# Performance work log

Hardware: AMD Instinct MI355X
Metric: run time of the kernel (lower is better)

## Reference

```python
import jax, jax.numpy as jnp
import numpy as np

B, S, D = 2, 2048, 2048
H = 16
NOPE, ROPE, DV = 128, 64, 128
DQK = NOPE + ROPE  # 192
QLR, KVLR = 1536, 512


def setup_inputs() -> dict:
    key = jax.random.key(0)
    ks = jax.random.split(key, 8)
    hidden_states = jax.random.normal(ks[0], (B, S, D), dtype=jnp.float32) * 0.02
    sequence_mask = jnp.ones((B, S), dtype=bool)
    # rotary frequencies (complex exponential split into cos/sin), theta=10000
    inv_freq = 1.0 / (10000.0 ** (np.arange(0, ROPE, 2, dtype=np.float32) / ROPE))
    angles = np.outer(np.arange(S, dtype=np.float32), inv_freq)  # [S, ROPE//2]
    freqs_cos = jnp.asarray(np.cos(angles), dtype=jnp.float32)
    freqs_sin = jnp.asarray(np.sin(angles), dtype=jnp.float32)
    def lin(k, fan_in, fan_out):
        return jax.random.normal(k, (fan_in, fan_out), dtype=jnp.float32) / np.sqrt(fan_in)
    return {
        'hidden_states': hidden_states,
        'sequence_mask': sequence_mask,
        'freqs_cos': freqs_cos,
        'freqs_sin': freqs_sin,
        'Wq_down': lin(ks[1], D, QLR),
        'Wkv_down': lin(ks[2], D, KVLR + ROPE),
        'Wq_up': lin(ks[3], QLR, H * DQK),
        'Wkv_up': lin(ks[4], KVLR, H * (DV + NOPE)),
        'Wo': lin(ks[5], H * DV, D),
    }


def _rmsnorm(x, eps=1e-5):
    return x * jax.lax.rsqrt(jnp.mean(x * x, axis=-1, keepdims=True) + eps)


def _apply_rope(x, cos, sin):
    # x: [B,S,H,d] with interleaved (real, imag) pairs; cos/sin: [S, d//2]
    b, s, h, d = x.shape
    xr = x.reshape(b, s, h, d // 2, 2)
    x0, x1 = xr[..., 0], xr[..., 1]
    c = cos[None, :s, None, :]
    sn = sin[None, :s, None, :]
    y = jnp.stack([x0 * c - x1 * sn, x0 * sn + x1 * c], axis=-1)
    return y.reshape(b, s, h, d)


def reference(hidden_states, sequence_mask, freqs_cos, freqs_sin,
              Wq_down, Wkv_down, Wq_up, Wkv_up, Wo):
    b, s, _ = hidden_states.shape
    # Q path: down-project -> rmsnorm -> up-project
    q_latent = _rmsnorm(hidden_states @ Wq_down)
    q = (q_latent @ Wq_up).reshape(b, s, H, DQK)
    q_nope, q_rope = q[..., :NOPE], q[..., NOPE:]
    q_rope = _apply_rope(q_rope, freqs_cos, freqs_sin)
    q = jnp.concatenate([q_rope, q_nope], axis=-1)  # [B,S,H,DQK]
    # KV path
    kvdr = hidden_states @ Wkv_down  # [B,S,KVLR+ROPE]
    kv_latent, k_rope = kvdr[..., :KVLR], kvdr[..., KVLR:]
    k_rope = _apply_rope(k_rope.reshape(b, s, 1, ROPE), freqs_cos, freqs_sin)
    k_rope = jnp.broadcast_to(k_rope, (b, s, H, ROPE))
    kv = _rmsnorm(kv_latent) @ Wkv_up  # [B,S,H*(NOPE+DV)]
    k_nope = kv[..., :H * NOPE].reshape(b, s, H, NOPE)
    v = kv[..., H * NOPE:].reshape(b, s, H, DV)
    k = jnp.concatenate([k_rope, k_nope], axis=-1)  # [B,S,H,DQK]
    # causal attention (flash_attn_varlen with full masks == per-batch causal)
    scale = 1.0 / np.sqrt(DQK)
    scores = jnp.einsum('bqhd,bkhd->bhqk', q, k) * scale
    causal = jnp.tril(jnp.ones((s, s), dtype=bool))
    mask = causal[None, None, :, :] & sequence_mask[:, None, None, :]
    scores = jnp.where(mask, scores, jnp.float32(-1e9))
    attn = jax.nn.softmax(scores, axis=-1)
    out = jnp.einsum('bhqk,bkhd->bqhd', attn, v).reshape(b, s, H * DV)
    return out @ Wo
```

## Files before the change

### kernel.cpp

```cpp
#include <hip/hip_runtime.h>
#include <math.h>


typedef unsigned short u16;
typedef __attribute__((ext_vector_type(8))) __bf16 bf16x8;
typedef __attribute__((ext_vector_type(4))) float f32x4;

#define DEV static __device__ __forceinline__

#if __has_builtin(__builtin_amdgcn_exp2f)
#define EXP2(x) __builtin_amdgcn_exp2f(x)
#else
#define EXP2(x) exp2f(x)
#endif

DEV float b2f(u16 v) { return __uint_as_float(((unsigned int)v) << 16); }
DEV u16 f2b(float f) {
  unsigned int u = __float_as_uint(f);
  u += 0x7fffu + ((u >> 16) & 1u);
  return (u16)(u >> 16);
}
DEV u16 f2b_hw(float f) {
  __bf16 h = (__bf16)f;
  u16 r;
  __builtin_memcpy(&r, &h, 2);
  return r;
}

DEV float waveReduceSum(float v) {
  #pragma unroll
  for (int o = 32; o > 0; o >>= 1) v += __shfl_down(v, o, 64);
  return v;
}

DEV void gld16(const u16* g, u16* l) {
  __builtin_amdgcn_global_load_lds((const __attribute__((address_space(1))) void*)g,
                                   (__attribute__((address_space(3))) void*)l, 16, 0, 0);
}

__global__ __launch_bounds__(256)
void cvt_f32_bf16(const float* __restrict__ in, u16* __restrict__ out, int n4) {
  int i = blockIdx.x * 256 + threadIdx.x;
  if (i < n4) {
    float4 v = reinterpret_cast<const float4*>(in)[i];
    ushort4 o;
    o.x = f2b(v.x); o.y = f2b(v.y); o.z = f2b(v.z); o.w = f2b(v.w);
    reinterpret_cast<ushort4*>(out)[i] = o;
  }
}

__global__ __launch_bounds__(256)
void transpose_all(const float* __restrict__ Wqd, const float* __restrict__ Wkvd,
                   const float* __restrict__ Wqu, const float* __restrict__ Wkvu,
                   const float* __restrict__ Wo,
                   u16* __restrict__ W13T, u16* __restrict__ WquT,
                   u16* __restrict__ WkvuT, u16* __restrict__ WoT) {
  __shared__ u16 tile[32][33];
  int n = blockIdx.x;
  const float* in; u16* out; int R, C, gx, local;
  if (n < 3072)       { in = Wqd;  out = W13T;                        R = 2048; C = 1536; gx = 48;  local = n; }
  else if (n < 4224)  { in = Wkvd; out = W13T + (size_t)1536 * 2048;  R = 2048; C = 576;  gx = 18;  local = n - 3072; }
  else if (n < 8832)  { in = Wqu;  out = WquT;                        R = 1536; C = 3072; gx = 96;  local = n - 4224; }
  else if (n < 10880) { in = Wkvu; out = WkvuT;                       R = 512;  C = 4096; gx = 128; local = n - 8832; }
  else                { in = Wo;   out = WoT;                         R = 2048; C = 2048; gx = 64;  local = n - 10880; }
  int c0 = (local % gx) * 32, r0 = (local / gx) * 32;
  for (int i = threadIdx.y; i < 32; i += 8)
    tile[i][threadIdx.x] = f2b(in[(size_t)(r0 + i) * C + c0 + threadIdx.x]);
  __syncthreads();
  for (int i = threadIdx.y; i < 32; i += 8)
    out[(size_t)(c0 + i) * R + r0 + threadIdx.x] = tile[threadIdx.x][i];
}

template<int OUT_BF16>
DEV void gemm8_body(const u16* __restrict__ A, const u16* __restrict__ BT, void* __restrict__ Cp,
                    int N, int K, int gx, int nwg, int orig,
                    u16 (*As)[8192], u16 (*Bs)[4096]) {
  const int tid = threadIdx.x;
  const int lane = tid & 63;
  const int wave = tid >> 6;
  const int wm = (wave >> 1) * 64;
  const int wn = (wave & 1) * 64;
  const int q = lane >> 4;
  const int l16 = lane & 15;

  const int cpx = nwg >> 3;
  const int swz = (orig & 7) * cpx + (orig >> 3);
  const int bm = (swz / gx) * 256;
  const int bn = (swz % gx) * 128;

  auto stageA = [&](int buf, int k0) {
    #pragma unroll
    for (int i = 0; i < 2; i++) {
      int ub = i * 512 + wave * 64;
      int u = ub + lane;
      int row = u >> 2;
      int kq = (u & 3) ^ ((u >> 3) & 3);
      gld16(A + (size_t)(bm + row) * K + k0 + kq * 8, As[buf] + ub * 8);
    }
  };
  auto stageB = [&](int buf, int k0) {
    int ub = wave * 64;
    int u = ub + lane;
    int row = u >> 2;
    int kq = (u & 3) ^ ((u >> 3) & 3);
    int rB = bn + row;
    if (rB >= N) rB = N - 1;
    gld16(BT + (size_t)rB * K + k0 + kq * 8, Bs[buf] + ub * 8);
  };

  f32x4 zero = {0.f, 0.f, 0.f, 0.f};
  f32x4 acc[4][4];
  #pragma unroll
  for (int i = 0; i < 4; i++)
    #pragma unroll
    for (int j = 0; j < 4; j++) acc[i][j] = zero;

  const int nt = K >> 5;
  stageA(0, 0);  stageB(0, 0);
  stageA(1, 32); stageB(1, 32);

  for (int t = 0; t < nt; ++t) {
    const int cur = t % 3;
    if (t + 1 < nt) asm volatile("s_waitcnt vmcnt(3)" ::: "memory");
    else            asm volatile("s_waitcnt vmcnt(0)" ::: "memory");
    __builtin_amdgcn_sched_barrier(0);
    __builtin_amdgcn_s_barrier();
    __builtin_amdgcn_sched_barrier(0);

    const u16* Ab = As[cur];
    const u16* Bb = Bs[cur];
    const int nxt = (t + 2) % 3;
    const bool pre = (t + 2) < nt;
    const int kpre = (t + 2) * 32;

    bf16x8 af[4], bfr[4];
    #pragma unroll
    for (int j = 0; j < 4; j++) {
      int rowA = wm + j * 16 + l16;
      af[j]  = *reinterpret_cast<const bf16x8*>(Ab + (((rowA) << 2) | (q ^ ((rowA >> 1) & 3))) * 8);
      int rowB = wn + j * 16 + l16;
      bfr[j] = *reinterpret_cast<const bf16x8*>(Bb + (((rowB) << 2) | (q ^ ((rowB >> 1) & 3))) * 8);
    }
    if (pre) { stageA(nxt, kpre); stageB(nxt, kpre); }
    __builtin_amdgcn_s_setprio(1);
    #pragma unroll
    for (int mt = 0; mt < 4; mt++)
      #pragma unroll
      for (int j = 0; j < 4; j++)
        acc[mt][j] = __builtin_amdgcn_mfma_f32_16x16x32_bf16(af[mt], bfr[j], acc[mt][j], 0, 0, 0);
    __builtin_amdgcn_s_setprio(0);
  }

  float* Cf = (float*)Cp;
  u16* Cb = (u16*)Cp;
  #pragma unroll
  for (int mt = 0; mt < 4; mt++) {
    #pragma unroll
    for (int j = 0; j < 4; j++) {
      int col = bn + wn + j * 16 + l16;
      if (col < N) {
        int row0 = bm + wm + mt * 16 + q * 4;
        #pragma unroll
        for (int r = 0; r < 4; r++) {
          size_t idx = (size_t)(row0 + r) * N + col;
          float v = acc[mt][j][r];
          if (OUT_BF16) Cb[idx] = f2b(v); else Cf[idx] = v;
        }
      }
    }
  }
}

template<int OUT_BF16>
__global__ __launch_bounds__(512, 4)
void gemm8(const u16* __restrict__ A, const u16* __restrict__ BT, void* __restrict__ Cp,
           int N, int K) {
  __shared__ __attribute__((aligned(16))) u16 As[3][8192];
  __shared__ __attribute__((aligned(16))) u16 Bs[3][4096];
  const int gx = gridDim.x;
  const int nwg = gx * gridDim.y;
  const int orig = blockIdx.y * gx + blockIdx.x;
  gemm8_body<OUT_BF16>(A, BT, Cp, N, K, gx, nwg, orig, As, Bs);
}

__global__ __launch_bounds__(512, 4)
void gemm_up2(const u16* __restrict__ qlat, const u16* __restrict__ WquT, u16* __restrict__ q2,
              const u16* __restrict__ kvl, const u16* __restrict__ WkvuT, u16* __restrict__ kvb) {
  __shared__ __attribute__((aligned(16))) u16 As[3][8192];
  __shared__ __attribute__((aligned(16))) u16 Bs[3][4096];
  int n = blockIdx.x;
  if (n < 384) gemm8_body<1>(qlat, WquT, q2, 3072, 1536, 24, 384, n, As, Bs);
  else         gemm8_body<1>(kvl, WkvuT, kvb, 4096, 512, 32, 512, n - 384, As, Bs);
}

__global__ __launch_bounds__(256)
void norm_split(const float* __restrict__ t13, const float* __restrict__ fc, const float* __restrict__ fs,
                u16* __restrict__ qlat, u16* __restrict__ kvl, u16* __restrict__ krope) {
  __shared__ float red[4];
  __shared__ float s_scale;
  int lane = threadIdx.x & 63, wid = threadIdx.x >> 6;
  if (blockIdx.x < 4096) {
    int row = blockIdx.x;
    const float* x = t13 + (size_t)row * 2112;
    float ss = 0.f;
    for (int i = threadIdx.x; i < 1536; i += 256) { float v = x[i]; ss += v * v; }
    ss = waveReduceSum(ss);
    if (lane == 0) red[wid] = ss;
    __syncthreads();
    if (threadIdx.x == 0)
      s_scale = rsqrtf((red[0] + red[1] + red[2] + red[3]) * (1.0f / 1536.0f) + 1e-5f);
    __syncthreads();
    float sc = s_scale;
    u16* o = qlat + (size_t)row * 1536;
    for (int i = threadIdx.x; i < 1536; i += 256) o[i] = f2b(x[i] * sc);
  } else {
    int row = blockIdx.x - 4096;
    int s = row & 2047;
    const float* x = t13 + (size_t)row * 2112 + 1536;
    float ss = 0.f;
    for (int i = threadIdx.x; i < 512; i += 256) { float v = x[i]; ss += v * v; }
    ss = waveReduceSum(ss);
    if (lane == 0) red[wid] = ss;
    __syncthreads();
    if (threadIdx.x == 0)
      s_scale = rsqrtf((red[0] + red[1] + red[2] + red[3]) * (1.0f / 512.0f) + 1e-5f);
    __syncthreads();
    float sc = s_scale;
    for (int i = threadIdx.x; i < 512; i += 256) kvl[(size_t)row * 512 + i] = f2b(x[i] * sc);
    if (threadIdx.x < 32) {
      int i = threadIdx.x;
      float cc = fc[s * 32 + i], sn = fs[s * 32 + i];
      float x0 = x[512 + 2 * i], x1 = x[512 + 2 * i + 1];
      krope[(size_t)row * 64 + 2 * i]     = f2b(x0 * cc - x1 * sn);
      krope[(size_t)row * 64 + 2 * i + 1] = f2b(x0 * sn + x1 * cc);
    }
  }
}

__global__ __launch_bounds__(256)
void rope_pack_q(const u16* __restrict__ q2, const float* __restrict__ fc, const float* __restrict__ fs,
                 u16* __restrict__ Q) {
  const float scale = 0.10411756711f;
  int bs = blockIdx.x;
  int b = bs >> 11, s = bs & 2047;
  __shared__ float c[32], sn[32];
  if (threadIdx.x < 32) {
    c[threadIdx.x] = fc[s * 32 + threadIdx.x];
    sn[threadIdx.x] = fs[s * 32 + threadIdx.x];
  }
  __syncthreads();
  const u16* qrow = q2 + (size_t)bs * 3072;
  for (int t = threadIdx.x; t < 512; t += 256) {
    int h = t >> 5, i = t & 31;
    float x0 = b2f(qrow[h * 192 + 128 + 2 * i]);
    float x1 = b2f(qrow[h * 192 + 128 + 2 * i + 1]);
    size_t base = ((size_t)(b * 16 + h) * 2048 + s) * 192;
    Q[base + 2 * i]     = f2b((x0 * c[i] - x1 * sn[i]) * scale);
    Q[base + 2 * i + 1] = f2b((x0 * sn[i] + x1 * c[i]) * scale);
  }
  for (int t = threadIdx.x; t < 2048; t += 256) {
    int h = t >> 7, j = t & 127;
    Q[((size_t)(b * 16 + h) * 2048 + s) * 192 + 64 + j] = f2b(b2f(qrow[h * 192 + j]) * scale);
  }
}

__global__ __launch_bounds__(256)
void assemble_kv2(const u16* __restrict__ kvb, const u16* __restrict__ krope,
                  u16* __restrict__ Kc, u16* __restrict__ Vt) {
  int ks = blockIdx.x;
  int bh = blockIdx.y;
  int b = bh >> 4, h = bh & 15;
  int t = threadIdx.x;
  if (t < 192) {
    int kq = t >> 3, sl = t & 7;
    int s = ks * 8 + sl;
    size_t bs = (size_t)(b * 2048 + s);
    uint4 v;
    if (kq < 8) v = *reinterpret_cast<const uint4*>(krope + bs * 64 + kq * 8);
    else        v = *reinterpret_cast<const uint4*>(kvb + bs * 4096 + h * 128 + (kq - 8) * 8);
    *reinterpret_cast<uint4*>(Kc + (((size_t)bh * 24 + kq) * 2048 + s) * 8) = v;
  }
  if (t < 128) {
    int dv = t;
    u16 tmp[8];
    #pragma unroll
    for (int j = 0; j < 8; j++) {
      int s = ks * 8 + j;
      tmp[j] = kvb[(size_t)(b * 2048 + s) * 4096 + 2048 + h * 128 + dv];
    }
    *reinterpret_cast<uint4*>(Vt + (((size_t)bh * 256 + ks) * 128 + dv) * 8) = *reinterpret_cast<uint4*>(tmp);
  }
}

__global__ __launch_bounds__(256, 2)
void flash_attn8(const u16* __restrict__ Q, const u16* __restrict__ Kc,
                 const u16* __restrict__ Vt, u16* __restrict__ O) {
  __shared__ __attribute__((aligned(16))) u16 Ks[2][24 * 64 * 8];
  __shared__ __attribute__((aligned(16))) u16 Vs[8 * 128 * 8];
  __shared__ __attribute__((aligned(16))) u16 Ps[4 * 16 * 72];

  const int blk = blockIdx.x;
  const int bh = ((blk & 7) << 2) | (blk >> 7);
  const int tpair = (blk >> 3) & 15;
  const int b = bh >> 4, h = bh & 15;
  const int tid = threadIdx.x, lane = tid & 63, wave = tid >> 6;
  const int quad = lane >> 4, l16 = lane & 15;
  u16* PsW = Ps + wave * 16 * 72;

  bf16x8 onesf;
  #pragma unroll
  for (int j = 0; j < 8; j++) onesf[j] = (l16 == 0) ? (__bf16)1.0f : (__bf16)0.0f;

  auto stageK = [&](u16* KsB, int kk) {
    #pragma unroll
    for (int ii = 0; ii < 6; ii++) {
      int kq = wave * 6 + ii;
      gld16(Kc + (((size_t)bh * 24 + kq) * 2048 + kk + lane) * 8, KsB + kq * 64 * 8);
    }
  };
  auto stageV = [&](int kk) {
    #pragma unroll
    for (int jj = 0; jj < 4; jj++) {
      int vc = wave * 4 + jj, kc = vc >> 1, dvh = vc & 1;
      gld16(Vt + (((size_t)bh * 256 + (kk >> 3) + kc) * 128 + dvh * 64 + lane) * 8,
            Vs + (kc * 128 + dvh * 64) * 8);
    }
  };

  for (int phase = 0; phase < 2; phase++) {
    const int qt = phase == 0 ? tpair : 31 - tpair;
    const int q0 = qt * 64;
    const int nk = (qt + 1) * 64;

    bf16x8 qf[6];
    {
      int qrow = q0 + wave * 16 + l16;
      const u16* qp = Q + ((size_t)bh * 2048 + qrow) * 192 + quad * 8;
      #pragma unroll
      for (int kc = 0; kc < 6; kc++)
        qf[kc] = *reinterpret_cast<const bf16x8*>(qp + kc * 32);
    }

    f32x4 zero = {0.f, 0.f, 0.f, 0.f};
    f32x4 oacc[9];
    #pragma unroll
    for (int nt = 0; nt < 9; nt++) oacc[nt] = zero;

    for (int k0 = 0; k0 < nk; k0 += 64) {
      const int cur = (k0 >> 6) & 1;
      const bool hasnext = (k0 + 64 < nk);

      __builtin_amdgcn_s_barrier();
      __builtin_amdgcn_sched_barrier(0);
      if (k0 == 0) stageK(Ks[0], 0);
      stageV(k0);
      if (hasnext) {
        stageK(Ks[cur ^ 1], k0 + 64);
        asm volatile("s_waitcnt vmcnt(10)" ::: "memory");
      } else {
        asm volatile("s_waitcnt vmcnt(4)" ::: "memory");
      }
      __builtin_amdgcn_sched_barrier(0);
      __builtin_amdgcn_s_barrier();
      __builtin_amdgcn_sched_barrier(0);

      const u16* KsC = Ks[cur];

      f32x4 sacc[4];
      #pragma unroll
      for (int nt = 0; nt < 4; nt++) sacc[nt] = zero;
      #pragma unroll
      for (int kc = 0; kc < 6; kc++) {
        #pragma unroll
        for (int nt = 0; nt < 4; nt++) {
          bf16x8 kb = *reinterpret_cast<const bf16x8*>(KsC + ((kc * 4 + quad) * 64 + nt * 16 + l16) * 8);
          sacc[nt] = __builtin_amdgcn_mfma_f32_16x16x32_bf16(qf[kc], kb, sacc[nt], 0, 0, 0);
        }
      }

      if (k0 + 63 <= q0 + wave * 16) {
        #pragma unroll
        for (int r = 0; r < 4; r++) {
          #pragma unroll
          for (int nt = 0; nt < 4; nt++) {
            float p = EXP2(sacc[nt][r]);
            PsW[(quad * 4 + r) * 72 + nt * 16 + l16] = f2b_hw(p);
          }
        }
      } else {
        #pragma unroll
        for (int r = 0; r < 4; r++) {
          int qrow_g = q0 + wave * 16 + quad * 4 + r;
          #pragma unroll
          for (int nt = 0; nt < 4; nt++) {
            int key = k0 + nt * 16 + l16;
            float e = EXP2(sacc[nt][r]);
            float p = (key <= qrow_g) ? e : 0.f;
            PsW[(quad * 4 + r) * 72 + nt * 16 + l16] = f2b_hw(p);
          }
        }
      }

      if (hasnext) asm volatile("s_waitcnt vmcnt(6)" ::: "memory");
      else         asm volatile("s_waitcnt vmcnt(0)" ::: "memory");
      __builtin_amdgcn_sched_barrier(0);
      __builtin_amdgcn_s_barrier();
      __builtin_amdgcn_sched_barrier(0);

      #pragma unroll
      for (int kcp = 0; kcp < 2; kcp++) {
        bf16x8 pa = *reinterpret_cast<const bf16x8*>(PsW + l16 * 72 + kcp * 32 + quad * 8);
        #pragma unroll
        for (int nt = 0; nt < 8; nt++) {
          bf16x8 vb = *reinterpret_cast<const bf16x8*>(Vs + ((kcp * 4 + quad) * 128 + nt * 16 + l16) * 8);
          oacc[nt] = __builtin_amdgcn_mfma_f32_16x16x32_bf16(pa, vb, oacc[nt], 0, 0, 0);
        }
        oacc[8] = __builtin_amdgcn_mfma_f32_16x16x32_bf16(pa, onesf, oacc[8], 0, 0, 0);
      }
    }

    #pragma unroll
    for (int r = 0; r < 4; r++) {
      float l = __shfl(oacc[8][r], lane & 48, 64);
      float inv = 1.0f / l;
      int s = q0 + wave * 16 + quad * 4 + r;
      #pragma unroll
      for (int nt = 0; nt < 8; nt++)
        O[((size_t)b * 2048 + s) * 2048 + h * 128 + nt * 16 + l16] = f2b(oacc[nt][r] * inv);
    }
  }
}

extern "C" void kernel_launch(void* const* d_in, const int* in_sizes, int n_in,
                              void* d_out, int out_size, void* d_ws, size_t ws_size,
                              hipStream_t stream) {
  (void)in_sizes; (void)n_in; (void)out_size; (void)ws_size;
  const float* hs   = (const float*)d_in[0];
  const float* fc   = (const float*)d_in[2];
  const float* fs   = (const float*)d_in[3];
  const float* Wqd  = (const float*)d_in[4];
  const float* Wkvd = (const float*)d_in[5];
  const float* Wqu  = (const float*)d_in[6];
  const float* Wkvu = (const float*)d_in[7];
  const float* Wo   = (const float*)d_in[8];

  char* ws = (char*)d_ws;
  size_t off = 0;
  auto alloc = [&](size_t bytes) { size_t o = off; off += (bytes + 255) & ~(size_t)255; return o; };
  const size_t oHS   = alloc(16777216);
  const size_t oRA   = alloc(16777216);
  const size_t oRB   = alloc(25165824);
  const size_t oRC   = alloc(12582912);
  const size_t oRD   = alloc(25165824);
  const size_t oRE   = alloc(34603008);
  const size_t oKVL  = alloc(4194304);
  const size_t oKR   = alloc(524288);
  const size_t oW13T  = alloc(8650752);
  const size_t oWquT  = alloc(9437184);
  const size_t oWkvuT = alloc(4194304);
  const size_t oWoT   = alloc(8388608);

  u16* hs_bf = (u16*)(ws + oHS);
  u16* Vt   = (u16*)(ws + oRA);
  u16* q2   = (u16*)(ws + oRB);
  u16* Kc   = (u16*)(ws + oRB);
  u16* qlat = (u16*)(ws + oRC);
  u16* Qb   = (u16*)(ws + oRD);
  float* t13 = (float*)(ws + oRE);
  u16* kvb  = (u16*)(ws + oRE);
  u16* attn_out = (u16*)(ws + oRE);
  u16* kvl  = (u16*)(ws + oKVL);
  u16* krope = (u16*)(ws + oKR);
  u16* W13T  = (u16*)(ws + oW13T);
  u16* WquT  = (u16*)(ws + oWquT);
  u16* WkvuT = (u16*)(ws + oWkvuT);
  u16* WoT   = (u16*)(ws + oWoT);

  cvt_f32_bf16<<<8192, 256, 0, stream>>>(hs, hs_bf, 2097152);
  transpose_all<<<14976, dim3(32, 8), 0, stream>>>(Wqd, Wkvd, Wqu, Wkvu, Wo, W13T, WquT, WkvuT, WoT);

  gemm8<0><<<dim3(17, 16), 512, 0, stream>>>(hs_bf, W13T, t13, 2112, 2048);
  norm_split<<<8192, 256, 0, stream>>>(t13, fc, fs, qlat, kvl, krope);
  gemm_up2<<<896, 512, 0, stream>>>(qlat, WquT, q2, kvl, WkvuT, kvb);
  rope_pack_q<<<4096, 256, 0, stream>>>(q2, fc, fs, Qb);
  assemble_kv2<<<dim3(256, 32), 256, 0, stream>>>(kvb, krope, Kc, Vt);
  flash_attn8<<<dim3(512), 256, 0, stream>>>(Qb, Kc, Vt, attn_out);
  gemm8<0><<<dim3(16, 16), 512, 0, stream>>>(attn_out, WoT, (float*)d_out, 2048, 2048);
}
```

Measured before the change: 412.9 us.

## Process both causal query tiles in one shared key loop in flash attention

Each block previously handled its two paired query tiles (short and long) one after the other, restaging K and V from global memory for each. The new kernel keeps Q fragments and output accumulators for both tiles in registers and walks the keys once. Each staged K/V tile feeds both tiles' MFMAs while the short tile is still active. This removes duplicate global loads and barrier rounds for the short tile, at the cost of roughly doubling accumulator and Q register use, which may hurt scheduling or cause spills.

```diff
diff --git a/kernel.cpp b/kernel.cpp
--- a/kernel.cpp
+++ b/kernel.cpp
@@ -293,7 +293,7 @@
 }
 
 __global__ __launch_bounds__(256, 2)
-void flash_attn8(const u16* __restrict__ Q, const u16* __restrict__ Kc,
+void flash_attn9(const u16* __restrict__ Q, const u16* __restrict__ Kc,
                  const u16* __restrict__ Vt, u16* __restrict__ O) {
   __shared__ __attribute__((aligned(16))) u16 Ks[2][24 * 64 * 8];
   __shared__ __attribute__((aligned(16))) u16 Vs[8 * 128 * 8];
@@ -307,6 +307,11 @@
   const int quad = lane >> 4, l16 = lane & 15;
   u16* PsW = Ps + wave * 16 * 72;
 
+  const int q0A = tpair * 64;
+  const int q0B = (31 - tpair) * 64;
+  const int nkA = q0A + 64;
+  const int nkB = q0B + 64;
+
   bf16x8 onesf;
   #pragma unroll
   for (int j = 0; j < 8; j++) onesf[j] = (l16 == 0) ? (__bf16)1.0f : (__bf16)0.0f;
@@ -327,106 +332,130 @@
     }
   };
 
-  for (int phase = 0; phase < 2; phase++) {
-    const int qt = phase == 0 ? tpair : 31 - tpair;
-    const int q0 = qt * 64;
-    const int nk = (qt + 1) * 64;
-
-    bf16x8 qf[6];
-    {
-      int qrow = q0 + wave * 16 + l16;
-      const u16* qp = Q + ((size_t)bh * 2048 + qrow) * 192 + quad * 8;
+  bf16x8 qf[2][6];
+  #pragma unroll
+  for (int s = 0; s < 2; s++) {
+    int qrow = (s ? q0B : q0A) + wave * 16 + l16;
+    const u16* qp = Q + ((size_t)bh * 2048 + qrow) * 192 + quad * 8;
+    #pragma unroll
+    for (int kc = 0; kc < 6; kc++)
+      qf[s][kc] = *reinterpret_cast<const bf16x8*>(qp + kc * 32);
+  }
+
+  f32x4 zero = {0.f, 0.f, 0.f, 0.f};
+  f32x4 oacc[2][9];
+  #pragma unroll
+  for (int s = 0; s < 2; s++)
+    #pragma unroll
+    for (int nt = 0; nt < 9; nt++) oacc[s][nt] = zero;
+
+  for (int k0 = 0; k0 < nkB; k0 += 64) {
+    const int cur = (k0 >> 6) & 1;
+    const bool hasnext = (k0 + 64 < nkB);
+    const bool aA = (k0 < nkA);
+
+    __builtin_amdgcn_s_barrier();
+    __builtin_amdgcn_sched_barrier(0);
+    if (k0 == 0) stageK(Ks[0], 0);
+    stageV(k0);
+    if (hasnext) {
+      stageK(Ks[cur ^ 1], k0 + 64);
+      asm volatile("s_waitcnt vmcnt(10)" ::: "memory");
+    } else {
+      asm volatile("s_waitcnt vmcnt(4)" ::: "memory");
+    }
+    __builtin_amdgcn_sched_barrier(0);
+    __builtin_amdgcn_s_barrier();
+    __builtin_amdgcn_sched_barrier(0);
+
+    const u16* KsC = Ks[cur];
+
+    f32x4 sacc[2][4];
+    #pragma unroll
+    for (int s = 0; s < 2; s++)
       #pragma unroll
-      for (int kc = 0; kc < 6; kc++)
-        qf[kc] = *reinterpret_cast<const bf16x8*>(qp + kc * 32);
-    }
-
-    f32x4 zero = {0.f, 0.f, 0.f, 0.f};
-    f32x4 oacc[9];
-    #pragma unroll
-    for (int nt = 0; nt < 9; nt++) oacc[nt] = zero;
-
-    for (int k0 = 0; k0 < nk; k0 += 64) {
-      const int cur = (k0 >> 6) & 1;
-      const bool hasnext = (k0 + 64 < nk);
-
-      __builtin_amdgcn_s_barrier();
-      __builtin_amdgcn_sched_barrier(0);
-      if (k0 == 0) stageK(Ks[0], 0);
-      stageV(k0);
-      if (hasnext) {
-        stageK(Ks[cur ^ 1], k0 + 64);
-        asm volatile("s_waitcnt vmcnt(10)" ::: "memory");
-      } else {
-        asm volatile("s_waitcnt vmcnt(4)" ::: "memory");
-      }
-      __builtin_amdgcn_sched_barrier(0);
-      __builtin_amdgcn_s_barrier();
-      __builtin_amdgcn_sched_barrier(0);
-
-      const u16* KsC = Ks[cur];
-
-      f32x4 sacc[4];
-      #pragma unroll
-      for (int nt = 0; nt < 4; nt++) sacc[nt] = zero;
+      for (int nt = 0; nt < 4; nt++) sacc[s][nt] = zero;
+    if (aA) {
       #pragma unroll
       for (int kc = 0; kc < 6; kc++) {
         #pragma unroll
         for (int nt = 0; nt < 4; nt++) {
           bf16x8 kb = *reinterpret_cast<const bf16x8*>(KsC + ((kc * 4 + quad) * 64 + nt * 16 + l16) * 8);
-          sacc[nt] = __builtin_amdgcn_mfma_f32_16x16x32_bf16(qf[kc], kb, sacc[nt], 0, 0, 0);
+          sacc[1][nt] = __builtin_amdgcn_mfma_f32_16x16x32_bf16(qf[1][kc], kb, sacc[1][nt], 0, 0, 0);
+          sacc[0][nt] = __builtin_amdgcn_mfma_f32_16x16x32_bf16(qf[0][kc], kb, sacc[0][nt], 0, 0, 0);
         }
       }
-
-      if (k0 + 63 <= q0 + wave * 16) {
+    } else {
+      #pragma unroll
+      for (int kc = 0; kc < 6; kc++) {
         #pragma unroll
-        for (int r = 0; r < 4; r++) {
+        for (int nt = 0; nt < 4; nt++) {
+          bf16x8 kb = *reinterpret_cast<const bf16x8*>(KsC + ((kc * 4 + quad) * 64 + nt * 16 + l16) * 8);
+          sacc[1][nt] = __builtin_amdgcn_mfma_f32_16x16x32_bf16(qf[1][kc], kb, sacc[1][nt], 0, 0, 0);
+        }
+      }
+    }
+
+    auto softmax = [&](int s, int q0s) {
+      if (k0 + 63 <= q0s + wave * 16) {
+        #pragma unroll
+        for (int r = 0; r < 4; r++)
           #pragma unroll
           for (int nt = 0; nt < 4; nt++) {
-            float p = EXP2(sacc[nt][r]);
+            float p = EXP2(sacc[s][nt][r]);
             PsW[(quad * 4 + r) * 72 + nt * 16 + l16] = f2b_hw(p);
           }
-        }
       } else {
         #pragma unroll
         for (int r = 0; r < 4; r++) {
-          int qrow_g = q0 + wave * 16 + quad * 4 + r;
+          int qrow_g = q0s + wave * 16 + quad * 4 + r;
           #pragma unroll
           for (int nt = 0; nt < 4; nt++) {
             int key = k0 + nt * 16 + l16;
-            float e = EXP2(sacc[nt][r]);
+            float e = EXP2(sacc[s][nt][r]);
             float p = (key <= qrow_g) ? e : 0.f;
             PsW[(quad * 4 + r) * 72 + nt * 16 + l16] = f2b_hw(p);
           }
         }
       }
-
-      if (hasnext) asm volatile("s_waitcnt vmcnt(6)" ::: "memory");
-      else         asm volatile("s_waitcnt vmcnt(0)" ::: "memory");
-      __builtin_amdgcn_sched_barrier(0);
-      __builtin_amdgcn_s_barrier();
-      __builtin_amdgcn_sched_barrier(0);
-
+    };
+    auto pv = [&](int s) {
       #pragma unroll
       for (int kcp = 0; kcp < 2; kcp++) {
         bf16x8 pa = *reinterpret_cast<const bf16x8*>(PsW + l16 * 72 + kcp * 32 + quad * 8);
         #pragma unroll
         for (int nt = 0; nt < 8; nt++) {
           bf16x8 vb = *reinterpret_cast<const bf16x8*>(Vs + ((kcp * 4 + quad) * 128 + nt * 16 + l16) * 8);
-          oacc[nt] = __builtin_amdgcn_mfma_f32_16x16x32_bf16(pa, vb, oacc[nt], 0, 0, 0);
+          oacc[s][nt] = __builtin_amdgcn_mfma_f32_16x16x32_bf16(pa, vb, oacc[s][nt], 0, 0, 0);
         }
-        oacc[8] = __builtin_amdgcn_mfma_f32_16x16x32_bf16(pa, onesf, oacc[8], 0, 0, 0);
+        oacc[s][8] = __builtin_amdgcn_mfma_f32_16x16x32_bf16(pa, onesf, oacc[s][8], 0, 0, 0);
       }
-    }
-
+    };
+
+    softmax(1, q0B);
+    if (hasnext) asm volatile("s_waitcnt vmcnt(6)" ::: "memory");
+    else         asm volatile("s_waitcnt vmcnt(0)" ::: "memory");
+    __builtin_amdgcn_sched_barrier(0);
+    __builtin_amdgcn_s_barrier();
+    __builtin_amdgcn_sched_barrier(0);
+    pv(1);
+    if (aA) {
+      softmax(0, q0A);
+      pv(0);
+    }
+  }
+
+  #pragma unroll
+  for (int s = 0; s < 2; s++) {
+    int q0s = s ? q0B : q0A;
     #pragma unroll
     for (int r = 0; r < 4; r++) {
-      float l = __shfl(oacc[8][r], lane & 48, 64);
+      float l = __shfl(oacc[s][8][r], lane & 48, 64);
       float inv = 1.0f / l;
-      int s = q0 + wave * 16 + quad * 4 + r;
+      int sr = q0s + wave * 16 + quad * 4 + r;
       #pragma unroll
       for (int nt = 0; nt < 8; nt++)
-        O[((size_t)b * 2048 + s) * 2048 + h * 128 + nt * 16 + l16] = f2b(oacc[nt][r] * inv);
+        O[((size_t)b * 2048 + sr) * 2048 + h * 128 + nt * 16 + l16] = f2b(oacc[s][nt][r] * inv);
     }
   }
 }
@@ -484,6 +513,6 @@
   gemm_up2<<<896, 512, 0, stream>>>(qlat, WquT, q2, kvl, WkvuT, kvb);
   rope_pack_q<<<4096, 256, 0, stream>>>(q2, fc, fs, Qb);
   assemble_kv2<<<dim3(256, 32), 256, 0, stream>>>(kvb, krope, Kc, Vt);
-  flash_attn8<<<dim3(512), 256, 0, stream>>>(Qb, Kc, Vt, attn_out);
+  flash_attn9<<<dim3(512), 256, 0, stream>>>(Qb, Kc, Vt, attn_out);
   gemm8<0><<<dim3(16, 16), 512, 0, stream>>>(attn_out, WoT, (float*)d_out, 2048, 2048);
 }
```

Result: no change. 409.0 us (-0.9%).
